# Optimization experiments

Measured on AMD Instinct MI355X. Metric: run time of the kernel, lower is better.

## Reference

```python
import jax, jax.numpy as jnp
import numpy as np

VOCAB_SIZE = 1024
EMBED_DIM = 64
Z_SHAPE = (64, 32, 32, EMBED_DIM)


def setup_inputs() -> dict:
    key = jax.random.key(0)
    kz, kc = jax.random.split(key)
    z = jax.random.normal(kz, Z_SHAPE, dtype=jnp.float32)
    codebook = jax.random.uniform(kc, (VOCAB_SIZE, EMBED_DIM), dtype=jnp.float32)
    return {"z": z, "codebook": codebook}


def reference(z, codebook):
    # Flatten all leading dims: [N, D]
    z_flat = jnp.reshape(z, (-1, EMBED_DIM))
    # Squared euclidean distance via expansion: |z|^2 + |c|^2 - 2 z.c
    d1 = jnp.sum(z_flat ** 2, axis=1, keepdims=True)      # [N, 1]
    d2 = jnp.sum(codebook ** 2, axis=1)                   # [V]
    d3 = 2.0 * jnp.dot(z_flat, codebook.T)                # [N, V]
    distances = d1 + d2 - d3                              # [N, V]
    tokens = jnp.argmin(distances, axis=1)                # [N]
    tokens = jnp.reshape(tokens, z.shape[:-1])            # [B, H, W]
    z_quantized = codebook[tokens]                        # [B, H, W, D]
    return (z_quantized, tokens, codebook)
```

## Files before the change

### kernel.cpp

```cpp
#include <hip/hip_runtime.h>
#include <float.h>

constexpr int D     = 64;
constexpr int V     = 1024;
constexpr int NROWS = 65536;
constexpr float MARGIN = 0.01f;

typedef _Float16 half8 __attribute__((ext_vector_type(8)));
typedef float    f32x4 __attribute__((ext_vector_type(4)));

__global__ __launch_bounds__(256) void vq_prep(
    const float* __restrict__ cb, _Float16* __restrict__ wsH,
    _Float16* __restrict__ wsL, float* __restrict__ c2,
    float* __restrict__ cbout, int* __restrict__ cnt) {
  const int gid = blockIdx.x * 256 + threadIdx.x;
  if (gid == 0) cnt[0] = 0;

  ((float4*)cbout)[gid] = ((const float4*)cb)[gid];

  if (gid < V) {
    const int cw = gid;
    const float* src = cb + (size_t)cw * D;
    float part = 0.f;
#pragma unroll
    for (int chunk = 0; chunk < 8; ++chunk) {
      float4 q0 = ((const float4*)(src + chunk * 8))[0];
      float4 q1 = ((const float4*)(src + chunk * 8))[1];
      float xs[8] = {q0.x, q0.y, q0.z, q0.w, q1.x, q1.y, q1.z, q1.w};
      half8 hh, hl;
#pragma unroll
      for (int e = 0; e < 8; ++e) {
        _Float16 hi = (_Float16)xs[e];
        hh[e] = hi;
        hl[e] = (_Float16)(xs[e] - (float)hi);
        part  = fmaf(xs[e], xs[e], part);
      }
      *(half8*)&wsH[((size_t)chunk * V + cw) * 8] = hh;
      *(half8*)&wsL[((size_t)chunk * V + cw) * 8] = hl;
    }
    c2[cw] = part;
  }
}

__global__ __launch_bounds__(256, 4) void vq_screen(
    const float* __restrict__ z, const float* __restrict__ cb,
    const _Float16* __restrict__ wsH, const _Float16* __restrict__ wsL,
    const float* __restrict__ c2g,
    float* __restrict__ zq, float* __restrict__ tok,
    int* __restrict__ cnt, int* __restrict__ list) {
  __shared__ __align__(16) _Float16 sBh[8][128][8];
  __shared__ __align__(16) _Float16 sBl[8][128][8];
  __shared__ __align__(16) float sC2a[1024];
  __shared__ int   sW[4][16];
  __shared__ int   sFlagRows[64];
  __shared__ int   sFlagCnt, sFlagBase;

  const int tid  = threadIdx.x;
  const int lane = tid & 63;
  const int wv   = tid >> 6;
  const int l15  = lane & 15;
  const int quad = lane >> 4;
  const int gw   = blockIdx.x * 4 + wv;
  const int rowbase = gw * 16;

  if (tid == 0) sFlagCnt = 0;

  half8 afh[2], afl[2];
  {
    const float* zr = z + (size_t)(rowbase + l15) * D;
#pragma unroll
    for (int h = 0; h < 2; ++h) {
      const float4* p = (const float4*)(zr + h * 32 + quad * 8);
      float4 q0 = p[0], q1 = p[1];
      float xs[8] = {q0.x, q0.y, q0.z, q0.w, q1.x, q1.y, q1.z, q1.w};
      half8 ah, al;
#pragma unroll
      for (int e = 0; e < 8; ++e) {
        _Float16 hi = (_Float16)xs[e];
        ah[e] = hi;
        al[e] = (_Float16)(xs[e] - (float)hi);
      }
      afh[h] = ah; afl[h] = al;
    }
  }

  float b1[4], b2[4]; int i1[4];
#pragma unroll
  for (int r = 0; r < 4; ++r) { b1[r] = FLT_MAX; b2[r] = FLT_MAX; i1[r] = 0; }

  {
    float4 qc = ((const float4*)c2g)[tid];
    *(float4*)&sC2a[tid * 4] = qc;
  }
#pragma unroll
  for (int i = 0; i < 8; ++i) {
    const int idx   = i * 256 + tid;
    const int seg   = idx >> 7;
    const int off   = idx & 127;
    const int chunk = seg & 7;
    const _Float16* srcb = (seg < 8) ? wsH : wsL;
    const half8 v = *(const half8*)&srcb[((size_t)chunk * V + off) * 8];
    if (seg < 8) *(half8*)&sBh[chunk][off][0] = v;
    else         *(half8*)&sBl[chunk][off][0] = v;
  }
  __syncthreads();

  for (int phase = 0; phase < 8; ++phase) {
    half8 pre[8];
    if (phase < 7) {
#pragma unroll
      for (int i = 0; i < 8; ++i) {
        const int idx   = i * 256 + tid;
        const int seg   = idx >> 7;
        const int off   = idx & 127;
        const int chunk = seg & 7;
        const _Float16* srcb = (seg < 8) ? wsH : wsL;
        pre[i] = *(const half8*)&srcb[((size_t)chunk * V + (phase + 1) * 128 + off) * 8];
      }
    }
#pragma unroll 2
    for (int tl = 0; tl < 8; ++tl) {
      const int cwl  = tl * 16 + l15;
      const int vcol = phase * 128 + cwl;
      const float c2v = sC2a[phase * 128 + cwl];
      half8 bh0 = *(const half8*)&sBh[quad][cwl][0];
      half8 bh1 = *(const half8*)&sBh[4 + quad][cwl][0];
      half8 bl0 = *(const half8*)&sBl[quad][cwl][0];
      half8 bl1 = *(const half8*)&sBl[4 + quad][cwl][0];
      f32x4 acc = {0.f, 0.f, 0.f, 0.f};
      acc = __builtin_amdgcn_mfma_f32_16x16x32_f16(afh[0], bh0, acc, 0, 0, 0);
      acc = __builtin_amdgcn_mfma_f32_16x16x32_f16(afh[1], bh1, acc, 0, 0, 0);
      acc = __builtin_amdgcn_mfma_f32_16x16x32_f16(afh[0], bl0, acc, 0, 0, 0);
      acc = __builtin_amdgcn_mfma_f32_16x16x32_f16(afh[1], bl1, acc, 0, 0, 0);
      acc = __builtin_amdgcn_mfma_f32_16x16x32_f16(afl[0], bh0, acc, 0, 0, 0);
      acc = __builtin_amdgcn_mfma_f32_16x16x32_f16(afl[1], bh1, acc, 0, 0, 0);
#pragma unroll
      for (int r = 0; r < 4; ++r) {
        float m0 = fmaf(-2.f, acc[r], c2v);
        bool  c0 = m0 < b1[r];
        b2[r] = fminf(b2[r], fmaxf(m0, b1[r]));
        b1[r] = c0 ? m0 : b1[r];
        i1[r] = c0 ? vcol : i1[r];
      }
    }
    __syncthreads();
    if (phase < 7) {
#pragma unroll
      for (int i = 0; i < 8; ++i) {
        const int idx   = i * 256 + tid;
        const int seg   = idx >> 7;
        const int off   = idx & 127;
        const int chunk = seg & 7;
        if (seg < 8) *(half8*)&sBh[chunk][off][0] = pre[i];
        else         *(half8*)&sBl[chunk][off][0] = pre[i];
      }
      __syncthreads();
    }
  }

#pragma unroll
  for (int r = 0; r < 4; ++r) {
    float v1 = b1[r], v2 = b2[r]; int ix = i1[r];
#pragma unroll
    for (int s = 1; s < 16; s <<= 1) {
      float ov1 = __shfl_xor(v1, s);
      float ov2 = __shfl_xor(v2, s);
      int   oix = __shfl_xor(ix, s);
      bool take = (ov1 < v1) || (ov1 == v1 && oix < ix);
      float worse = take ? v1 : ov1;
      v2 = fminf(fminf(v2, ov2), worse);
      v1 = take ? ov1 : v1;
      ix = take ? oix : ix;
    }
    b1[r] = v1; b2[r] = v2; i1[r] = ix;
  }

  if (l15 == 0) {
#pragma unroll
    for (int r = 0; r < 4; ++r) {
      int rl = quad * 4 + r;
      sW[wv][rl] = i1[r];
      if (b2[r] - b1[r] < MARGIN) {
        int s = atomicAdd(&sFlagCnt, 1);
        sFlagRows[s] = rowbase + rl;
      }
    }
  }
  __syncthreads();
  if (tid == 0 && sFlagCnt > 0) sFlagBase = atomicAdd(cnt, sFlagCnt);
  __syncthreads();
  if (tid < sFlagCnt) list[sFlagBase + tid] = sFlagRows[tid];

  if (tid < 64) tok[blockIdx.x * 64 + tid] = (float)sW[tid >> 4][tid & 15];

#pragma unroll
  for (int i = 0; i < 4; ++i) {
    int cid = i * 256 + tid;
    int r = cid >> 4, seg = cid & 15;
    int widx = sW[r >> 4][r & 15];
    float4 val = *(const float4*)(cb + (size_t)widx * D + seg * 4);
    *(float4*)(zq + (size_t)(blockIdx.x * 64 + r) * D + seg * 4) = val;
  }
}

__global__ __launch_bounds__(256) void vq_fallback(
    const float* __restrict__ z, const float* __restrict__ cb,
    const int* __restrict__ cnt, const int* __restrict__ list,
    float* __restrict__ zq, float* __restrict__ tok) {
  __shared__ float sv[256];
  __shared__ int   si[256];
  const int t = threadIdx.x;
  const int n = cnt[0];
  for (int it = blockIdx.x; it < n; it += gridDim.x) {
    int row = __builtin_amdgcn_readfirstlane(list[it]);
    const float* zr = z + (size_t)row * D;
    float zreg[D];
#pragma unroll
    for (int i = 0; i < D / 4; ++i) {
      float4 q = ((const float4*)zr)[i];
      zreg[4 * i] = q.x; zreg[4 * i + 1] = q.y; zreg[4 * i + 2] = q.z; zreg[4 * i + 3] = q.w;
    }
    float d1 = 0.f;
#pragma unroll
    for (int i = 0; i < D; ++i) d1 = fmaf(zreg[i], zreg[i], d1);
    float best = FLT_MAX; int bidx = 0;
    for (int c = 0; c < 4; ++c) {
      int v = t + 256 * c;
      const float* cp = cb + (size_t)v * D;
      float acc = 0.f, cc = 0.f;
#pragma unroll
      for (int dd = 0; dd < D; ++dd) {
        acc = fmaf(zreg[dd], cp[dd], acc);
        cc  = fmaf(cp[dd], cp[dd], cc);
      }
      float dist = (d1 + cc) - 2.f * acc;
      if (dist < best) { best = dist; bidx = v; }
    }
    sv[t] = best; si[t] = bidx;
    __syncthreads();
    for (int s = 128; s > 0; s >>= 1) {
      if (t < s) {
        float v2 = sv[t + s]; int i2 = si[t + s];
        if (v2 < sv[t] || (v2 == sv[t] && i2 < si[t])) { sv[t] = v2; si[t] = i2; }
      }
      __syncthreads();
    }
    int win = si[0];
    if (t == 0) tok[row] = (float)win;
    if (t < 16) {
      float4 q = ((const float4*)(cb + (size_t)win * D))[t];
      ((float4*)(zq + (size_t)row * D))[t] = q;
    }
    __syncthreads();
  }
}

extern "C" void kernel_launch(void* const* d_in, const int* in_sizes, int n_in,
                              void* d_out, int out_size, void* d_ws, size_t ws_size,
                              hipStream_t stream) {
  const float* z  = (const float*)d_in[0];
  const float* cb = (const float*)d_in[1];

  float* out = (float*)d_out;
  float* zq  = out;
  float* tok = out + (size_t)NROWS * D;
  float* cbo = tok + NROWS;

  char* wsb = (char*)d_ws;
  _Float16* wsH  = (_Float16*)(wsb + 0);
  _Float16* wsL  = (_Float16*)(wsb + 131072);
  float*    c2   = (float*)(wsb + 262144);
  int*      cnt  = (int*)(wsb + 266240);
  int*      list = (int*)(wsb + 266496);

  vq_prep<<<64, 256, 0, stream>>>(cb, wsH, wsL, c2, cbo, cnt);
  vq_screen<<<1024, 256, 0, stream>>>(z, cb, wsH, wsL, c2, zq, tok, cnt, list);
  vq_fallback<<<1024, 256, 0, stream>>>(z, cb, cnt, list, zq, tok);
}
```

Measured before the change: 130.6 us.

## Double-buffer codebook tiles in LDS with half-size phases and one barrier

Splits the codebook into 16 tiles of 64 codewords instead of 8 tiles of 128 and ping-pongs between two LDS buffers. The register prefetch of the next tile is written into the other buffer right after compute, so each phase needs one __syncthreads instead of two. The aim is less barrier stall and better overlap of global loads with MFMA work, at the same LDS footprint. In exchange the number of phases doubles, so there are more loop iterations and the per-phase prefetch latency has less compute to hide behind.

After: 130.9 us. No clear change (+0.2%).

```diff
diff --git a/kernel.cpp b/kernel.cpp
--- a/kernel.cpp
+++ b/kernel.cpp
@@ -48,8 +48,8 @@
     const float* __restrict__ c2g,
     float* __restrict__ zq, float* __restrict__ tok,
     int* __restrict__ cnt, int* __restrict__ list) {
-  __shared__ __align__(16) _Float16 sBh[8][128][8];
-  __shared__ __align__(16) _Float16 sBl[8][128][8];
+  __shared__ __align__(16) _Float16 sBh[2][8][64][8];
+  __shared__ __align__(16) _Float16 sBl[2][8][64][8];
   __shared__ __align__(16) float sC2a[1024];
   __shared__ int   sW[4][16];
   __shared__ int   sFlagRows[64];
@@ -93,40 +93,42 @@
     *(float4*)&sC2a[tid * 4] = qc;
   }
 #pragma unroll
-  for (int i = 0; i < 8; ++i) {
+  for (int i = 0; i < 4; ++i) {
     const int idx   = i * 256 + tid;
-    const int seg   = idx >> 7;
-    const int off   = idx & 127;
+    const int seg   = idx >> 6;
+    const int off   = idx & 63;
     const int chunk = seg & 7;
     const _Float16* srcb = (seg < 8) ? wsH : wsL;
     const half8 v = *(const half8*)&srcb[((size_t)chunk * V + off) * 8];
-    if (seg < 8) *(half8*)&sBh[chunk][off][0] = v;
-    else         *(half8*)&sBl[chunk][off][0] = v;
+    if (seg < 8) *(half8*)&sBh[0][chunk][off][0] = v;
+    else         *(half8*)&sBl[0][chunk][off][0] = v;
   }
   __syncthreads();
 
-  for (int phase = 0; phase < 8; ++phase) {
-    half8 pre[8];
-    if (phase < 7) {
-#pragma unroll
-      for (int i = 0; i < 8; ++i) {
+  for (int hp = 0; hp < 16; ++hp) {
+    const int cur = hp & 1;
+    const int nxt = cur ^ 1;
+    half8 pre[4];
+    if (hp < 15) {
+#pragma unroll
+      for (int i = 0; i < 4; ++i) {
         const int idx   = i * 256 + tid;
-        const int seg   = idx >> 7;
-        const int off   = idx & 127;
+        const int seg   = idx >> 6;
+        const int off   = idx & 63;
         const int chunk = seg & 7;
         const _Float16* srcb = (seg < 8) ? wsH : wsL;
-        pre[i] = *(const half8*)&srcb[((size_t)chunk * V + (phase + 1) * 128 + off) * 8];
-      }
-    }
-#pragma unroll 2
-    for (int tl = 0; tl < 8; ++tl) {
+        pre[i] = *(const half8*)&srcb[((size_t)chunk * V + (hp + 1) * 64 + off) * 8];
+      }
+    }
+#pragma unroll
+    for (int tl = 0; tl < 4; ++tl) {
       const int cwl  = tl * 16 + l15;
-      const int vcol = phase * 128 + cwl;
-      const float c2v = sC2a[phase * 128 + cwl];
-      half8 bh0 = *(const half8*)&sBh[quad][cwl][0];
-      half8 bh1 = *(const half8*)&sBh[4 + quad][cwl][0];
-      half8 bl0 = *(const half8*)&sBl[quad][cwl][0];
-      half8 bl1 = *(const half8*)&sBl[4 + quad][cwl][0];
+      const int vcol = hp * 64 + cwl;
+      const float c2v = sC2a[hp * 64 + cwl];
+      half8 bh0 = *(const half8*)&sBh[cur][quad][cwl][0];
+      half8 bh1 = *(const half8*)&sBh[cur][4 + quad][cwl][0];
+      half8 bl0 = *(const half8*)&sBl[cur][quad][cwl][0];
+      half8 bl1 = *(const half8*)&sBl[cur][4 + quad][cwl][0];
       f32x4 acc = {0.f, 0.f, 0.f, 0.f};
       acc = __builtin_amdgcn_mfma_f32_16x16x32_f16(afh[0], bh0, acc, 0, 0, 0);
       acc = __builtin_amdgcn_mfma_f32_16x16x32_f16(afh[1], bh1, acc, 0, 0, 0);
@@ -143,19 +145,18 @@
         i1[r] = c0 ? vcol : i1[r];
       }
     }
+    if (hp < 15) {
+#pragma unroll
+      for (int i = 0; i < 4; ++i) {
+        const int idx   = i * 256 + tid;
+        const int seg   = idx >> 6;
+        const int off   = idx & 63;
+        const int chunk = seg & 7;
+        if (seg < 8) *(half8*)&sBh[nxt][chunk][off][0] = pre[i];
+        else         *(half8*)&sBl[nxt][chunk][off][0] = pre[i];
+      }
+    }
     __syncthreads();
-    if (phase < 7) {
-#pragma unroll
-      for (int i = 0; i < 8; ++i) {
-        const int idx   = i * 256 + tid;
-        const int seg   = idx >> 7;
-        const int off   = idx & 127;
-        const int chunk = seg & 7;
-        if (seg < 8) *(half8*)&sBh[chunk][off][0] = pre[i];
-        else         *(half8*)&sBl[chunk][off][0] = pre[i];
-      }
-      __syncthreads();
-    }
   }
 
 #pragma unroll
```
